# Kernel optimization log

Measured on AMD Instinct MI355X. Metric: run time of the kernel, lower is better.

The kernel has to match this reference:

```python
import jax, jax.numpy as jnp
import numpy as np

B, N, DIM = 8, 1024, 1024
HEADS, DIM_HEAD = 16, 64
INNER = HEADS * DIM_HEAD  # 1024
SCALE = DIM_HEAD ** -0.5


def setup_inputs() -> dict:
    key = jax.random.key(0)
    ks = jax.random.split(key, 7)
    x = jax.random.normal(ks[0], (B, N, DIM), dtype=jnp.float32)
    context = jax.random.normal(ks[1], (B, N, DIM), dtype=jnp.float32)
    lengths = jax.random.randint(ks[2], (B,), 1, N + 1, dtype=jnp.int32)
    # Linear weights stored as (in, out); scaled like torch default init
    Wq = jax.random.normal(ks[3], (DIM, INNER), dtype=jnp.float32) * (DIM ** -0.5)
    Wkv = jax.random.normal(ks[4], (DIM, 2 * INNER), dtype=jnp.float32) * (DIM ** -0.5)
    Wout = jax.random.normal(ks[5], (INNER, DIM), dtype=jnp.float32) * (INNER ** -0.5)
    bout = jnp.zeros((DIM,), dtype=jnp.float32)
    return {"x": x, "context": context, "lengths": lengths,
            "Wq": Wq, "Wkv": Wkv, "Wout": Wout, "bout": bout}


def reference(x, context, lengths, Wq, Wkv, Wout, bout):
    b, n, _ = x.shape
    h, d = HEADS, DIM_HEAD
    q = x @ Wq                       # [b, n, h*d]
    kv = context @ Wkv               # [b, n, 2*h*d]
    k, v = jnp.split(kv, 2, axis=-1)

    def split_heads(t):
        return t.reshape(b, n, h, d).transpose(0, 2, 1, 3)  # [b, h, n, d]

    q, k, v = split_heads(q), split_heads(k), split_heads(v)
    dots = jnp.einsum('bhid,bhjd->bhij', q, k) * SCALE       # [b, h, n, n]
    # mask over key axis j: valid where j < lengths[b]
    mask = jnp.arange(n)[None, :] < lengths[:, None]         # [b, n]
    mask_value = -jnp.finfo(dots.dtype).max
    dots = jnp.where(mask[:, None, None, :], dots, mask_value)
    attn = jax.nn.softmax(dots, axis=-1)
    out = jnp.einsum('bhij,bhjd->bhid', attn, v)             # [b, h, n, d]
    out = out.transpose(0, 2, 1, 3).reshape(b, n, h * d)     # [b, n, h*d]
    return out @ Wout + bout
```

## Files before the change

kernel.cpp:

```cpp
#include <hip/hip_runtime.h>
#include <hip/hip_bf16.h>
#include <math.h>

typedef __attribute__((ext_vector_type(4))) float f32x4;
typedef __attribute__((ext_vector_type(8))) short bf16x8;

#define DEVI __device__ __forceinline__
#define GLBP(p) ((const __attribute__((address_space(1))) void*)(p))
#define LDSP(p) ((__attribute__((address_space(3))) void*)(p))

DEVI unsigned short f2b(float x) {
    __hip_bfloat16 b = __float2bfloat16(x);
    return *reinterpret_cast<unsigned short*>(&b);
}

__global__ void cast_f32_to_bf16(const float* __restrict__ in,
                                 unsigned short* __restrict__ out, int n) {
    int stride = gridDim.x * blockDim.x;
    for (int i = blockIdx.x * blockDim.x + threadIdx.x; i * 4 < n; i += stride) {
        float4 v = reinterpret_cast<const float4*>(in)[i];
        ushort4 o;
        o.x = f2b(v.x); o.y = f2b(v.y); o.z = f2b(v.z); o.w = f2b(v.w);
        reinterpret_cast<ushort4*>(out)[i] = o;
    }
}

__global__ void transpose_cast(const float* __restrict__ in,
                               unsigned short* __restrict__ out, int R, int C) {
    __shared__ float t[32][33];
    int bc = blockIdx.x * 32, br = blockIdx.y * 32;
    int x = threadIdx.x, y = threadIdx.y;
#pragma unroll
    for (int j = 0; j < 32; j += 8)
        t[y + j][x] = in[(size_t)(br + y + j) * C + bc + x];
    __syncthreads();
#pragma unroll
    for (int j = 0; j < 32; j += 8)
        out[(size_t)(bc + y + j) * R + br + x] = f2b(t[x][y + j]);
}

template<int OUTF32>
__global__ __launch_bounds__(256, 2)
void gemm_bt(const unsigned short* __restrict__ A,
             const unsigned short* __restrict__ B,
             void* __restrict__ Cp, const float* __restrict__ bias,
             int M, int N, int K) {
    __shared__ unsigned short As[128 * 32];
    __shared__ unsigned short Bs[128 * 32];
    const int tid  = threadIdx.x;
    const int wave = tid >> 6;
    const int lane = tid & 63;
    const int nbn  = N >> 7;
    const int bm   = blockIdx.x / nbn;
    const int bn   = blockIdx.x - bm * nbn;

    const int lr  = lane & 15;
    const int lk8 = (lane >> 4) << 3;
    const int wr  = (wave >> 1) * 64;
    const int wc  = (wave & 1) * 64;

    const unsigned short* ag = A + (size_t)(bm * 128 + (tid >> 2)) * K + ((tid & 3) << 3);
    const unsigned short* bg = B + (size_t)(bn * 128 + (tid >> 2)) * K + ((tid & 3) << 3);
    unsigned short* asd = As + wave * 512;
    unsigned short* bsd = Bs + wave * 512;

    f32x4 acc[4][4];
#pragma unroll
    for (int m = 0; m < 4; ++m)
#pragma unroll
        for (int n = 0; n < 4; ++n)
            acc[m][n] = (f32x4){0.f, 0.f, 0.f, 0.f};

    for (int k0 = 0; k0 < K; k0 += 32) {
        __builtin_amdgcn_global_load_lds(GLBP(ag + k0),                    LDSP(asd),        16, 0, 0);
        __builtin_amdgcn_global_load_lds(GLBP(ag + (size_t)64 * K + k0),   LDSP(asd + 2048), 16, 0, 0);
        __builtin_amdgcn_global_load_lds(GLBP(bg + k0),                    LDSP(bsd),        16, 0, 0);
        __builtin_amdgcn_global_load_lds(GLBP(bg + (size_t)64 * K + k0),   LDSP(bsd + 2048), 16, 0, 0);
        __syncthreads();
        bf16x8 af[4], bfr[4];
#pragma unroll
        for (int m = 0; m < 4; ++m)
            af[m] = *reinterpret_cast<const bf16x8*>(&As[(wr + m * 16 + lr) * 32 + lk8]);
#pragma unroll
        for (int n = 0; n < 4; ++n)
            bfr[n] = *reinterpret_cast<const bf16x8*>(&Bs[(wc + n * 16 + lr) * 32 + lk8]);
#pragma unroll
        for (int m = 0; m < 4; ++m)
#pragma unroll
            for (int n = 0; n < 4; ++n)
                acc[m][n] = __builtin_amdgcn_mfma_f32_16x16x32_bf16(af[m], bfr[n], acc[m][n], 0, 0, 0);
        __syncthreads();
    }

    const int rb = (lane >> 4) << 2;
    if (OUTF32) {
        float* C = reinterpret_cast<float*>(Cp);
#pragma unroll
        for (int m = 0; m < 4; ++m)
#pragma unroll
            for (int n = 0; n < 4; ++n) {
                const int col = bn * 128 + wc + n * 16 + lr;
                const float bv = bias[col];
#pragma unroll
                for (int r = 0; r < 4; ++r) {
                    const int row = bm * 128 + wr + m * 16 + rb + r;
                    C[(size_t)row * N + col] = acc[m][n][r] + bv;
                }
            }
    } else {
        unsigned short* C = reinterpret_cast<unsigned short*>(Cp);
#pragma unroll
        for (int m = 0; m < 4; ++m)
#pragma unroll
            for (int n = 0; n < 4; ++n) {
                const int col = bn * 128 + wc + n * 16 + lr;
#pragma unroll
                for (int r = 0; r < 4; ++r) {
                    const int row = bm * 128 + wr + m * 16 + rb + r;
                    C[(size_t)row * N + col] = f2b(acc[m][n][r]);
                }
            }
    }
}

__global__ __launch_bounds__(256, 2)
void attn_fused(const unsigned short* __restrict__ Q,
                const unsigned short* __restrict__ KV,
                const int* __restrict__ lengths,
                unsigned short* __restrict__ O) {
    __shared__ unsigned short Kl[64 * 72];
    __shared__ unsigned short Vt[64 * 72];
    __shared__ unsigned short Pl[4][16 * 72];

    const int tid  = threadIdx.x;
    const int wave = tid >> 6;
    const int lane = tid & 63;
    const int qt = blockIdx.x & 15;
    const int bh = blockIdx.x >> 4;
    const int b  = bh >> 4;
    const int h  = bh & 15;
    const int L  = lengths[b];

    const int lr  = lane & 15;
    const int lk8 = (lane >> 4) << 3;
    const int rb  = (lane >> 4) << 2;

    const size_t qrow = (size_t)(b * 1024 + qt * 64 + wave * 16 + lr);
    bf16x8 qf[2];
    qf[0] = *reinterpret_cast<const bf16x8*>(&Q[qrow * 1024 + h * 64 + lk8]);
    qf[1] = *reinterpret_cast<const bf16x8*>(&Q[qrow * 1024 + h * 64 + 32 + lk8]);

    f32x4 oacc[4];
#pragma unroll
    for (int nd = 0; nd < 4; ++nd) oacc[nd] = (f32x4){0.f, 0.f, 0.f, 0.f};
    float mrun[4] = {-3.0e38f, -3.0e38f, -3.0e38f, -3.0e38f};
    float lrun[4] = {0.f, 0.f, 0.f, 0.f};

    const int ntiles = (L + 63) >> 6;
    for (int t = 0; t < ntiles; ++t) {
        const int j0 = t * 64;
        __syncthreads();
#pragma unroll
        for (int rep = 0; rep < 2; ++rep) {
            const int idx  = rep * 256 + tid;
            const int key  = idx >> 3;
            const int dseg = (idx & 7) << 3;
            const size_t krow = (size_t)(b * 1024 + j0 + key) * 2048 + h * 64;
            bf16x8 kv = *reinterpret_cast<const bf16x8*>(&KV[krow + dseg]);
            *reinterpret_cast<bf16x8*>(&Kl[key * 72 + dseg]) = kv;
            bf16x8 vv = *reinterpret_cast<const bf16x8*>(&KV[krow + 1024 + dseg]);
#pragma unroll
            for (int j = 0; j < 8; ++j)
                Vt[(dseg + j) * 72 + key] = (unsigned short)vv[j];
        }
        __syncthreads();

        f32x4 sacc[4];
#pragma unroll
        for (int n = 0; n < 4; ++n) sacc[n] = (f32x4){0.f, 0.f, 0.f, 0.f};
#pragma unroll
        for (int n = 0; n < 4; ++n) {
            bf16x8 kf0 = *reinterpret_cast<const bf16x8*>(&Kl[(n * 16 + lr) * 72 + lk8]);
            bf16x8 kf1 = *reinterpret_cast<const bf16x8*>(&Kl[(n * 16 + lr) * 72 + 32 + lk8]);
            sacc[n] = __builtin_amdgcn_mfma_f32_16x16x32_bf16(qf[0], kf0, sacc[n], 0, 0, 0);
            sacc[n] = __builtin_amdgcn_mfma_f32_16x16x32_bf16(qf[1], kf1, sacc[n], 0, 0, 0);
        }

        float sv[4][4];
#pragma unroll
        for (int n = 0; n < 4; ++n)
#pragma unroll
            for (int r = 0; r < 4; ++r) {
                const int key = j0 + n * 16 + lr;
                sv[n][r] = (key < L) ? sacc[n][r] * 0.125f : -3.0e38f;
            }

        float tmax[4], alpha[4], psum[4];
#pragma unroll
        for (int r = 0; r < 4; ++r) {
            float tm = fmaxf(fmaxf(sv[0][r], sv[1][r]), fmaxf(sv[2][r], sv[3][r]));
#pragma unroll
            for (int off = 1; off < 16; off <<= 1)
                tm = fmaxf(tm, __shfl_xor(tm, off));
            tmax[r] = tm;
            const float mn = fmaxf(mrun[r], tm);
            alpha[r] = __expf(mrun[r] - mn);
            mrun[r] = mn;
            psum[r] = 0.f;
        }
        float pv[4][4];
#pragma unroll
        for (int n = 0; n < 4; ++n)
#pragma unroll
            for (int r = 0; r < 4; ++r) {
                const float p = __expf(sv[n][r] - mrun[r]);
                pv[n][r] = p;
                psum[r] += p;
            }
#pragma unroll
        for (int r = 0; r < 4; ++r) {
#pragma unroll
            for (int off = 1; off < 16; off <<= 1)
                psum[r] += __shfl_xor(psum[r], off);
            lrun[r] = lrun[r] * alpha[r] + psum[r];
        }
#pragma unroll
        for (int nd = 0; nd < 4; ++nd)
#pragma unroll
            for (int r = 0; r < 4; ++r)
                oacc[nd][r] *= alpha[r];

#pragma unroll
        for (int n = 0; n < 4; ++n)
#pragma unroll
            for (int r = 0; r < 4; ++r)
                Pl[wave][(rb + r) * 72 + n * 16 + lr] = f2b(pv[n][r]);
        __syncthreads();

#pragma unroll
        for (int nd = 0; nd < 4; ++nd) {
#pragma unroll
            for (int kk = 0; kk < 2; ++kk) {
                bf16x8 pf = *reinterpret_cast<const bf16x8*>(&Pl[wave][lr * 72 + kk * 32 + lk8]);
                bf16x8 vf = *reinterpret_cast<const bf16x8*>(&Vt[(nd * 16 + lr) * 72 + kk * 32 + lk8]);
                oacc[nd] = __builtin_amdgcn_mfma_f32_16x16x32_bf16(pf, vf, oacc[nd], 0, 0, 0);
            }
        }
    }

    const size_t orow = (size_t)(b * 1024 + qt * 64 + wave * 16);
#pragma unroll
    for (int r = 0; r < 4; ++r) {
        const float inv = 1.0f / lrun[r];
#pragma unroll
        for (int nd = 0; nd < 4; ++nd)
            O[(orow + rb + r) * 1024 + h * 64 + nd * 16 + lr] = f2b(oacc[nd][r] * inv);
    }
}

extern "C" void kernel_launch(void* const* d_in, const int* in_sizes, int n_in,
                              void* d_out, int out_size, void* d_ws, size_t ws_size,
                              hipStream_t stream) {
    const float* x    = (const float*)d_in[0];
    const float* ctx  = (const float*)d_in[1];
    const int*   len  = (const int*)d_in[2];
    const float* Wq   = (const float*)d_in[3];
    const float* Wkv  = (const float*)d_in[4];
    const float* Wout = (const float*)d_in[5];
    const float* bout = (const float*)d_in[6];
    float* out = (float*)d_out;

    char* w = (char*)d_ws;
    unsigned short* xb   = (unsigned short*)w; w += (size_t)8192 * 1024 * 2;
    unsigned short* cb   = (unsigned short*)w; w += (size_t)8192 * 1024 * 2;
    unsigned short* qb   = (unsigned short*)w; w += (size_t)8192 * 1024 * 2;
    unsigned short* kvb  = (unsigned short*)w; w += (size_t)8192 * 2048 * 2;
    unsigned short* aob  = (unsigned short*)w; w += (size_t)8192 * 1024 * 2;
    unsigned short* wqt  = (unsigned short*)w; w += (size_t)1024 * 1024 * 2;
    unsigned short* wkvt = (unsigned short*)w; w += (size_t)2048 * 1024 * 2;
    unsigned short* wot  = (unsigned short*)w; w += (size_t)1024 * 1024 * 2;

    cast_f32_to_bf16<<<2048, 256, 0, stream>>>(x,   xb, 8192 * 1024);
    cast_f32_to_bf16<<<2048, 256, 0, stream>>>(ctx, cb, 8192 * 1024);
    dim3 tb(32, 8);
    transpose_cast<<<dim3(32, 32), tb, 0, stream>>>(Wq,   wqt,  1024, 1024);
    transpose_cast<<<dim3(64, 32), tb, 0, stream>>>(Wkv,  wkvt, 1024, 2048);
    transpose_cast<<<dim3(32, 32), tb, 0, stream>>>(Wout, wot,  1024, 1024);

    gemm_bt<0><<<512,  256, 0, stream>>>(xb, wqt,  (void*)qb,  nullptr, 8192, 1024, 1024);
    gemm_bt<0><<<1024, 256, 0, stream>>>(cb, wkvt, (void*)kvb, nullptr, 8192, 2048, 1024);
    attn_fused<<<2048, 256, 0, stream>>>(qb, kvb, len, aob);
    gemm_bt<1><<<512,  256, 0, stream>>>(aob, wot, (void*)out, bout, 8192, 1024, 1024);
}
```

Before: 307.0 us.

## Read K fragments directly from global memory, drop K LDS staging, swizzle block order

K tiles are no longer staged in shared memory. Each wave loads its MFMA K fragments straight from global memory, and the first barrier per tile is removed. V is loaded into registers before the QK MFMAs and transposed into LDS afterwards, so its latency overlaps with compute. A block-index swizzle changes which batch/head blocks run together, meant to improve L2 reuse of K/V. The trade-off is that every wave now issues redundant global K reads instead of sharing one LDS copy.

```diff
diff --git a/kernel.cpp b/kernel.cpp
--- a/kernel.cpp
+++ b/kernel.cpp
@@ -128,22 +128,25 @@
                 const unsigned short* __restrict__ KV,
                 const int* __restrict__ lengths,
                 unsigned short* __restrict__ O) {
-    __shared__ unsigned short Kl[64 * 72];
     __shared__ unsigned short Vt[64 * 72];
     __shared__ unsigned short Pl[4][16 * 72];
 
     const int tid  = threadIdx.x;
     const int wave = tid >> 6;
     const int lane = tid & 63;
-    const int qt = blockIdx.x & 15;
-    const int bh = blockIdx.x >> 4;
+    const int swz = (blockIdx.x & 7) * 256 + (blockIdx.x >> 3);
+    const int qt = swz & 15;
+    const int bh = swz >> 4;
     const int b  = bh >> 4;
     const int h  = bh & 15;
     const int L  = lengths[b];
 
     const int lr  = lane & 15;
-    const int lk8 = (lane >> 4) << 3;
-    const int rb  = (lane >> 4) << 2;
+    const int g   = lane >> 4;
+    const int lk8 = g << 3;
+    const int rb  = g << 2;
+
+    const size_t kvbase = (size_t)(b * 1024) * 2048 + h * 64;
 
     const size_t qrow = (size_t)(b * 1024 + qt * 64 + wave * 16 + lr);
     bf16x8 qf[2];
@@ -160,30 +163,33 @@
     for (int t = 0; t < ntiles; ++t) {
         const int j0 = t * 64;
         __syncthreads();
+
+        bf16x8 vv[2];
 #pragma unroll
         for (int rep = 0; rep < 2; ++rep) {
-            const int idx  = rep * 256 + tid;
-            const int key  = idx >> 3;
-            const int dseg = (idx & 7) << 3;
-            const size_t krow = (size_t)(b * 1024 + j0 + key) * 2048 + h * 64;
-            bf16x8 kv = *reinterpret_cast<const bf16x8*>(&KV[krow + dseg]);
-            *reinterpret_cast<bf16x8*>(&Kl[key * 72 + dseg]) = kv;
-            bf16x8 vv = *reinterpret_cast<const bf16x8*>(&KV[krow + 1024 + dseg]);
-#pragma unroll
-            for (int j = 0; j < 8; ++j)
-                Vt[(dseg + j) * 72 + key] = (unsigned short)vv[j];
-        }
-        __syncthreads();
+            const int dseg = ((rep * 4 + wave) & 7) << 3;
+            vv[rep] = *reinterpret_cast<const bf16x8*>(
+                &KV[kvbase + (size_t)(j0 + lane) * 2048 + 1024 + dseg]);
+        }
 
         f32x4 sacc[4];
 #pragma unroll
         for (int n = 0; n < 4; ++n) sacc[n] = (f32x4){0.f, 0.f, 0.f, 0.f};
 #pragma unroll
         for (int n = 0; n < 4; ++n) {
-            bf16x8 kf0 = *reinterpret_cast<const bf16x8*>(&Kl[(n * 16 + lr) * 72 + lk8]);
-            bf16x8 kf1 = *reinterpret_cast<const bf16x8*>(&Kl[(n * 16 + lr) * 72 + 32 + lk8]);
+            const unsigned short* kp = &KV[kvbase + (size_t)(j0 + n * 16 + lr) * 2048 + lk8];
+            bf16x8 kf0 = *reinterpret_cast<const bf16x8*>(kp);
+            bf16x8 kf1 = *reinterpret_cast<const bf16x8*>(kp + 32);
             sacc[n] = __builtin_amdgcn_mfma_f32_16x16x32_bf16(qf[0], kf0, sacc[n], 0, 0, 0);
             sacc[n] = __builtin_amdgcn_mfma_f32_16x16x32_bf16(qf[1], kf1, sacc[n], 0, 0, 0);
+        }
+
+#pragma unroll
+        for (int rep = 0; rep < 2; ++rep) {
+            const int dseg = ((rep * 4 + wave) & 7) << 3;
+#pragma unroll
+            for (int j = 0; j < 8; ++j)
+                Vt[(dseg + j) * 72 + lane] = (unsigned short)vv[rep][j];
         }
 
         float sv[4][4];
@@ -195,14 +201,13 @@
                 sv[n][r] = (key < L) ? sacc[n][r] * 0.125f : -3.0e38f;
             }
 
-        float tmax[4], alpha[4], psum[4];
+        float alpha[4], psum[4];
 #pragma unroll
         for (int r = 0; r < 4; ++r) {
             float tm = fmaxf(fmaxf(sv[0][r], sv[1][r]), fmaxf(sv[2][r], sv[3][r]));
 #pragma unroll
             for (int off = 1; off < 16; off <<= 1)
                 tm = fmaxf(tm, __shfl_xor(tm, off));
-            tmax[r] = tm;
             const float mn = fmaxf(mrun[r], tm);
             alpha[r] = __expf(mrun[r] - mn);
             mrun[r] = mn;
@@ -235,16 +240,17 @@
 #pragma unroll
             for (int r = 0; r < 4; ++r)
                 Pl[wave][(rb + r) * 72 + n * 16 + lr] = f2b(pv[n][r]);
+
         __syncthreads();
 
+        bf16x8 pf0 = *reinterpret_cast<const bf16x8*>(&Pl[wave][lr * 72 + lk8]);
+        bf16x8 pf1 = *reinterpret_cast<const bf16x8*>(&Pl[wave][lr * 72 + 32 + lk8]);
 #pragma unroll
         for (int nd = 0; nd < 4; ++nd) {
-#pragma unroll
-            for (int kk = 0; kk < 2; ++kk) {
-                bf16x8 pf = *reinterpret_cast<const bf16x8*>(&Pl[wave][lr * 72 + kk * 32 + lk8]);
-                bf16x8 vf = *reinterpret_cast<const bf16x8*>(&Vt[(nd * 16 + lr) * 72 + kk * 32 + lk8]);
-                oacc[nd] = __builtin_amdgcn_mfma_f32_16x16x32_bf16(pf, vf, oacc[nd], 0, 0, 0);
-            }
+            bf16x8 vf0 = *reinterpret_cast<const bf16x8*>(&Vt[(nd * 16 + lr) * 72 + lk8]);
+            bf16x8 vf1 = *reinterpret_cast<const bf16x8*>(&Vt[(nd * 16 + lr) * 72 + 32 + lk8]);
+            oacc[nd] = __builtin_amdgcn_mfma_f32_16x16x32_bf16(pf0, vf0, oacc[nd], 0, 0, 0);
+            oacc[nd] = __builtin_amdgcn_mfma_f32_16x16x32_bf16(pf1, vf1, oacc[nd], 0, 0, 0);
         }
     }
 
```

Measured after the change: 386.3 us. 1.26x slower.
